# Kernel tuning notes

Hardware: AMD Instinct MI355X
Metric: run time of the kernel (lower is better)

## Reference

```python
import jax, jax.numpy as jnp
import numpy as np

N_QUBITS = 10
BATCH = 16384
Q_DEPTH = 2


def _apply_1q_shared(state, U, q):
    # state: [B, 2, 2, ..., 2]; U: [2, 2] complex, acting on wire q
    state = jnp.moveaxis(state, 1 + q, -1)
    state = jnp.einsum('b...i,ji->b...j', state, U)
    return jnp.moveaxis(state, -1, 1 + q)


def _apply_ry_batched(state, angles, q):
    # per-sample RY(angle) on wire q; angles: [B] float
    c = jnp.cos(angles * 0.5).astype(jnp.complex64)
    s = jnp.sin(angles * 0.5).astype(jnp.complex64)
    U = jnp.stack([jnp.stack([c, -s], -1), jnp.stack([s, c], -1)], -2)  # [B,2,2]
    state = jnp.moveaxis(state, 1 + q, -1)
    state = jnp.einsum('b...i,bji->b...j', state, U)
    return jnp.moveaxis(state, -1, 1 + q)


def _rot_matrix(phi, theta, omega):
    # PennyLane Rot = RZ(omega) @ RY(theta) @ RZ(phi)
    c = jnp.cos(theta * 0.5)
    s = jnp.sin(theta * 0.5)
    m00 = jnp.exp(-0.5j * (phi + omega)) * c
    m01 = -jnp.exp(0.5j * (phi - omega)) * s
    m10 = jnp.exp(-0.5j * (phi - omega)) * s
    m11 = jnp.exp(0.5j * (phi + omega)) * c
    return jnp.stack([jnp.stack([m00, m01]), jnp.stack([m10, m11])]).astype(jnp.complex64)


def _apply_cnot(state, c, t):
    st = jnp.moveaxis(state, (1 + c, 1 + t), (1, 2))  # [B, ctrl, tgt, ...]
    st = jnp.stack([st[:, 0], st[:, 1, ::-1]], axis=1)  # flip target where ctrl=1
    return jnp.moveaxis(st, (1, 2), (1 + c, 1 + t))


def setup_inputs() -> dict:
    key = jax.random.key(0)
    k1, k2 = jax.random.split(key)
    x = jax.random.uniform(k1, (BATCH, N_QUBITS), dtype=jnp.float32) * np.pi
    q_weights = 0.01 * jax.random.normal(k2, (Q_DEPTH, N_QUBITS, 3), dtype=jnp.float32)
    return {"x": x, "q_weights": q_weights}


def reference(x, q_weights) -> jnp.ndarray:
    B, n = x.shape
    L = q_weights.shape[0]
    # |0...0> statevector, batched: [B] + [2]*n (axis q <-> wire q, wire 0 most significant)
    state = jnp.zeros((B, 2 ** n), jnp.complex64).at[:, 0].set(1.0)
    state = state.reshape((B,) + (2,) * n)
    # AngleEmbedding(rotation='Y')
    for q in range(n):
        state = _apply_ry_batched(state, x[:, q], q)
    # StronglyEntanglingLayers: Rot on each wire, then ring of CNOTs with range (l % (n-1)) + 1
    for l in range(L):
        for q in range(n):
            U = _rot_matrix(q_weights[l, q, 0], q_weights[l, q, 1], q_weights[l, q, 2])
            state = _apply_1q_shared(state, U, q)
        r = (l % (n - 1)) + 1
        for q in range(n):
            state = _apply_cnot(state, q, (q + r) % n)
    probs = jnp.abs(state.reshape(B, 2 ** n)) ** 2  # [B, 2^n]
    bits = (np.arange(2 ** n)[:, None] >> (n - 1 - np.arange(n))[None, :]) & 1
    signs = jnp.asarray(1.0 - 2.0 * bits, jnp.float32)  # [2^n, n], PauliZ eigenvalues
    return (probs @ signs).astype(jnp.float32)  # [B, n] expvals
```

## Files before the change

### kernel.cpp

```cpp
#include <hip/hip_runtime.h>

#define DEVINL __device__ __forceinline__

struct GC { int laneXor, regXor, rowL, rowR; };
struct Circ { GC g[20]; int sgnL[10], sgnR[10]; };

constexpr Circ build_circ() {
    Circ c{};
    unsigned A[10] = {};
    for (int i = 0; i < 10; ++i) A[i] = 1u << i;
    for (int w = 0; w < 10; ++w) {
        int pos = 9 - w;
        unsigned m = 1u << pos;
        c.g[w] = GC{ int(m >> 4), int(m & 15u), int(m >> 4), int(m & 15u) };
    }
    for (int q = 0; q < 10; ++q) { int pc = 9 - q, pt = 9 - ((q + 1) % 10); A[pt] ^= A[pc]; }
    unsigned M[10] = {}, Inv[10] = {};
    for (int i = 0; i < 10; ++i) { M[i] = A[i]; Inv[i] = 1u << i; }
    for (int col = 0; col < 10; ++col) {
        int piv = col;
        while (!((M[piv] >> col) & 1u)) ++piv;
        unsigned tm = M[col]; M[col] = M[piv]; M[piv] = tm;
        unsigned ti = Inv[col]; Inv[col] = Inv[piv]; Inv[piv] = ti;
        for (int r = 0; r < 10; ++r)
            if (r != col && ((M[r] >> col) & 1u)) { M[r] ^= M[col]; Inv[r] ^= Inv[col]; }
    }
    for (int w = 0; w < 10; ++w) {
        int pos = 9 - w;
        unsigned m = 0;
        for (int i = 0; i < 10; ++i) m |= ((Inv[i] >> pos) & 1u) << i;
        unsigned row = A[pos];
        c.g[10 + w] = GC{ int(m >> 4), int(m & 15u), int(row >> 4), int(row & 15u) };
    }
    for (int q = 0; q < 10; ++q) { int pc = 9 - q, pt = 9 - ((q + 2) % 10); A[pt] ^= A[pc]; }
    for (int q = 0; q < 10; ++q) { unsigned row = A[9 - q]; c.sgnL[q] = int(row >> 4); c.sgnR[q] = int(row & 15u); }
    return c;
}

constexpr Circ CC = build_circ();

DEVINL float csign(float v, int s) {
    return __int_as_float(__float_as_int(v) ^ (s << 31));
}

template<int XOR>
DEVINL float lx(float v, int lane) {
    int x = __float_as_int(v);
    int r;
    if constexpr (XOR == 1)      r = __builtin_amdgcn_update_dpp(0, x, 0xB1, 0xF, 0xF, true);
    else if constexpr (XOR == 2) r = __builtin_amdgcn_update_dpp(0, x, 0x4E, 0xF, 0xF, true);
    else if constexpr (XOR == 3) r = __builtin_amdgcn_update_dpp(0, x, 0x1B, 0xF, 0xF, true);
    else if constexpr (XOR < 32) r = __builtin_amdgcn_ds_swizzle(x, 0x1F | (XOR << 10));
    else                         r = __builtin_amdgcn_ds_bpermute((lane ^ XOR) << 2, x);
    return __int_as_float(r);
}

template<int G>
DEVINL void gates(float (&ar)[16], float (&ai)[16], const float* mats, int lane) {
    if constexpr (G < 20) {
        constexpr GC gc = CC.g[G];
        float fAr = mats[G * 4 + 0];
        float fAi = mats[G * 4 + 1];
        float fBr = mats[G * 4 + 2];
        float fBi = mats[G * 4 + 3];
        int sL = __popc(unsigned(lane & gc.rowL)) & 1;
        fAi = csign(fAi, sL);
        fBr = csign(fBr, sL);
        float br_[16], bi_[16];
        if constexpr (gc.laneXor == 0) {
            #pragma unroll
            for (int r = 0; r < 16; ++r) { br_[r] = ar[r ^ gc.regXor]; bi_[r] = ai[r ^ gc.regXor]; }
        } else {
            #pragma unroll
            for (int r = 0; r < 16; ++r) {
                br_[r] = lx<gc.laneXor>(ar[r ^ gc.regXor], lane);
                bi_[r] = lx<gc.laneXor>(ai[r ^ gc.regXor], lane);
            }
        }
        #pragma unroll
        for (int r = 0; r < 16; ++r) {
            const int cR = __builtin_popcount(unsigned(gc.rowR & r)) & 1;
            float a_r = ar[r], a_i = ai[r], b_r = br_[r], b_i = bi_[r];
            float nr, ni;
            if (!cR) {
                nr = fAr * a_r - fAi * a_i + fBr * b_r - fBi * b_i;
                ni = fAr * a_i + fAi * a_r + fBr * b_i + fBi * b_r;
            } else {
                nr = fAr * a_r + fAi * a_i - fBr * b_r - fBi * b_i;
                ni = fAr * a_i - fAi * a_r - fBr * b_i + fBi * b_r;
            }
            ar[r] = nr; ai[r] = ni;
        }
        gates<G + 1>(ar, ai, mats, lane);
    }
}

__global__ __launch_bounds__(256) void qsim(const float* __restrict__ x,
                                            const float* __restrict__ qw,
                                            float* __restrict__ out, int B) {
    __shared__ float sm[80];
    {
        int g = threadIdx.x;
        if (g < 20) {
            float phi = qw[g * 3 + 0], th = qw[g * 3 + 1], om = qw[g * 3 + 2];
            float c = cosf(0.5f * th), s = sinf(0.5f * th);
            float apo = 0.5f * (phi + om), amo = 0.5f * (phi - om);
            sm[g * 4 + 0] =  cosf(apo) * c;
            sm[g * 4 + 1] = -sinf(apo) * c;
            sm[g * 4 + 2] = -cosf(amo) * s;
            sm[g * 4 + 3] = -sinf(amo) * s;
        }
    }
    __syncthreads();

    int lane = threadIdx.x & 63;
    int b = __builtin_amdgcn_readfirstlane(blockIdx.x * 4 + (threadIdx.x >> 6));
    if (b >= B) return;

    const float* xb = x + b * 10;
    float f0r[10], f0i[10], f1r[10], f1i[10];
    #pragma unroll
    for (int w = 0; w < 10; ++w) {
        float h = 0.5f * xb[w];
        float s = __sinf(h), c = __cosf(h);
        float m0 = sm[w * 4 + 0], m1 = sm[w * 4 + 1], m2 = sm[w * 4 + 2], m3 = sm[w * 4 + 3];
        f0r[w] =  m0 * c + m2 * s;
        f0i[w] =  m1 * c + m3 * s;
        f1r[w] = -m2 * c + m0 * s;
        f1i[w] =  m3 * c - m1 * s;
    }

    float lfr, lfi;
    {
        int bit = lane & 1;
        lfr = bit ? f1r[5] : f0r[5];
        lfi = bit ? f1i[5] : f0i[5];
    }
    #pragma unroll
    for (int jj = 1; jj < 6; ++jj) {
        int w = 5 - jj;
        int bit = (lane >> jj) & 1;
        float pr = bit ? f1r[w] : f0r[w];
        float pi = bit ? f1i[w] : f0i[w];
        float nr = lfr * pr - lfi * pi;
        float ni = lfr * pi + lfi * pr;
        lfr = nr; lfi = ni;
    }
    float t01r[4], t01i[4], t23r[4], t23i[4];
    #pragma unroll
    for (int v = 0; v < 4; ++v) {
        float ar9 = (v & 1) ? f1r[9] : f0r[9], ai9 = (v & 1) ? f1i[9] : f0i[9];
        float ar8 = (v >> 1) ? f1r[8] : f0r[8], ai8 = (v >> 1) ? f1i[8] : f0i[8];
        t01r[v] = ar9 * ar8 - ai9 * ai8;
        t01i[v] = ar9 * ai8 + ai9 * ar8;
        float ar7 = (v & 1) ? f1r[7] : f0r[7], ai7 = (v & 1) ? f1i[7] : f0i[7];
        float ar6 = (v >> 1) ? f1r[6] : f0r[6], ai6 = (v >> 1) ? f1i[6] : f0i[6];
        t23r[v] = ar7 * ar6 - ai7 * ai6;
        t23i[v] = ar7 * ai6 + ai7 * ar6;
    }
    float g4r[4], g4i[4];
    #pragma unroll
    for (int v = 0; v < 4; ++v) {
        g4r[v] = lfr * t01r[v] - lfi * t01i[v];
        g4i[v] = lfr * t01i[v] + lfi * t01r[v];
    }
    float ar[16], ai[16];
    #pragma unroll
    for (int r = 0; r < 16; ++r) {
        ar[r] = g4r[r & 3] * t23r[r >> 2] - g4i[r & 3] * t23i[r >> 2];
        ai[r] = g4r[r & 3] * t23i[r >> 2] + g4i[r & 3] * t23r[r >> 2];
    }

    gates<10>(ar, ai, sm, lane);

    float prob[16];
    #pragma unroll
    for (int r = 0; r < 16; ++r) prob[r] = ar[r] * ar[r] + ai[r] * ai[r];

    float e[10];
    #pragma unroll
    for (int q = 0; q < 10; ++q) {
        float t = 0.f;
        #pragma unroll
        for (int r = 0; r < 16; ++r) {
            const int neg = __builtin_popcount(unsigned(CC.sgnR[q] & r)) & 1;
            t = neg ? (t - prob[r]) : (t + prob[r]);
        }
        int sl = __popc(unsigned(lane & CC.sgnL[q])) & 1;
        e[q] = csign(t, sl);
    }
    #pragma unroll
    for (int q = 0; q < 10; ++q) {
        e[q] += lx<1>(e[q], lane);
        e[q] += lx<2>(e[q], lane);
        e[q] += lx<4>(e[q], lane);
        e[q] += lx<8>(e[q], lane);
        e[q] += lx<16>(e[q], lane);
        e[q] += lx<32>(e[q], lane);
    }
    float v = e[0];
    #pragma unroll
    for (int q = 1; q < 10; ++q) v = (lane == q) ? e[q] : v;
    if (lane < 10) out[b * 10 + lane] = v;
}

extern "C" void kernel_launch(void* const* d_in, const int* in_sizes, int n_in,
                              void* d_out, int out_size, void* d_ws, size_t ws_size,
                              hipStream_t stream) {
    const float* x  = (const float*)d_in[0];
    const float* qw = (const float*)d_in[1];
    float* out = (float*)d_out;
    int B = in_sizes[0] / 10;
    int blocks = (B + 3) / 4;
    hipLaunchKernelGGL(qsim, dim3(blocks), dim3(256), 0, stream, x, qw, out, B);
}
```

Baseline: 95.30 us.

## Pack statevector amplitudes as fp16 pairs and apply gates with fdot2

```diff
diff --git a/kernel.cpp b/kernel.cpp
--- a/kernel.cpp
+++ b/kernel.cpp
@@ -1,6 +1,8 @@
 #include <hip/hip_runtime.h>
 
 #define DEVINL __device__ __forceinline__
+
+typedef _Float16 h2_t __attribute__((ext_vector_type(2)));
 
 struct GC { int laneXor, regXor, rowL, rowR; };
 struct Circ { GC g[20]; int sgnL[10], sgnR[10]; };
@@ -43,72 +45,79 @@
     return __int_as_float(__float_as_int(v) ^ (s << 31));
 }
 
+DEVINL int pk(float a, float b) {
+    return __builtin_bit_cast(int, __builtin_amdgcn_cvt_pkrtz(a, b));
+}
+DEVINL float fdot2(int p, int v, float acc) {
+    return __builtin_amdgcn_fdot2(__builtin_bit_cast(h2_t, p), __builtin_bit_cast(h2_t, v), acc, false);
+}
+
 template<int XOR>
-DEVINL float lx(float v, int lane) {
-    int x = __float_as_int(v);
-    int r;
-    if constexpr (XOR == 1)      r = __builtin_amdgcn_update_dpp(0, x, 0xB1, 0xF, 0xF, true);
-    else if constexpr (XOR == 2) r = __builtin_amdgcn_update_dpp(0, x, 0x4E, 0xF, 0xF, true);
-    else if constexpr (XOR == 3) r = __builtin_amdgcn_update_dpp(0, x, 0x1B, 0xF, 0xF, true);
-    else if constexpr (XOR < 32) r = __builtin_amdgcn_ds_swizzle(x, 0x1F | (XOR << 10));
-    else                         r = __builtin_amdgcn_ds_bpermute((lane ^ XOR) << 2, x);
-    return __int_as_float(r);
+DEVINL int lxi(int x, int lane) {
+    if constexpr (XOR == 1)      return __builtin_amdgcn_update_dpp(0, x, 0xB1, 0xF, 0xF, true);
+    else if constexpr (XOR == 2) return __builtin_amdgcn_update_dpp(0, x, 0x4E, 0xF, 0xF, true);
+    else if constexpr (XOR == 3) return __builtin_amdgcn_update_dpp(0, x, 0x1B, 0xF, 0xF, true);
+    else if constexpr (XOR < 32) return __builtin_amdgcn_ds_swizzle(x, 0x1F | (XOR << 10));
+    else                         return __builtin_amdgcn_ds_bpermute((lane ^ XOR) << 2, x);
+}
+template<int XOR>
+DEVINL float lxf(float v, int lane) {
+    return __int_as_float(lxi<XOR>(__float_as_int(v), lane));
 }
 
 template<int G>
-DEVINL void gates(float (&ar)[16], float (&ai)[16], const float* mats, int lane) {
+DEVINL void gates(int (&a)[16], const int* smP, int lane) {
     if constexpr (G < 20) {
         constexpr GC gc = CC.g[G];
-        float fAr = mats[G * 4 + 0];
-        float fAi = mats[G * 4 + 1];
-        float fBr = mats[G * 4 + 2];
-        float fBi = mats[G * 4 + 3];
         int sL = __popc(unsigned(lane & gc.rowL)) & 1;
-        fAi = csign(fAi, sL);
-        fBr = csign(fBr, sL);
-        float br_[16], bi_[16];
+        int p1 = smP[G * 4 + 0] ^ (sL << 31);
+        int p2 = smP[G * 4 + 1] ^ (sL << 15);
+        int p3 = smP[G * 4 + 2] ^ (sL << 15);
+        int p4 = smP[G * 4 + 3] ^ (sL << 31);
+        int q1 = p1 ^ (int)0x80000000;
+        int q2 = p2 ^ 0x8000;
+        int q3 = p3 ^ 0x8000;
+        int q4 = p4 ^ (int)0x80000000;
+        int b_[16];
         if constexpr (gc.laneXor == 0) {
             #pragma unroll
-            for (int r = 0; r < 16; ++r) { br_[r] = ar[r ^ gc.regXor]; bi_[r] = ai[r ^ gc.regXor]; }
+            for (int r = 0; r < 16; ++r) b_[r] = a[r ^ gc.regXor];
         } else {
             #pragma unroll
-            for (int r = 0; r < 16; ++r) {
-                br_[r] = lx<gc.laneXor>(ar[r ^ gc.regXor], lane);
-                bi_[r] = lx<gc.laneXor>(ai[r ^ gc.regXor], lane);
-            }
+            for (int r = 0; r < 16; ++r) b_[r] = lxi<gc.laneXor>(a[r ^ gc.regXor], lane);
         }
         #pragma unroll
         for (int r = 0; r < 16; ++r) {
             const int cR = __builtin_popcount(unsigned(gc.rowR & r)) & 1;
-            float a_r = ar[r], a_i = ai[r], b_r = br_[r], b_i = bi_[r];
-            float nr, ni;
-            if (!cR) {
-                nr = fAr * a_r - fAi * a_i + fBr * b_r - fBi * b_i;
-                ni = fAr * a_i + fAi * a_r + fBr * b_i + fBi * b_r;
-            } else {
-                nr = fAr * a_r + fAi * a_i - fBr * b_r - fBi * b_i;
-                ni = fAr * a_i - fAi * a_r - fBr * b_i + fBi * b_r;
-            }
-            ar[r] = nr; ai[r] = ni;
-        }
-        gates<G + 1>(ar, ai, mats, lane);
+            float nr = fdot2(cR ? q1 : p1, a[r], fdot2(cR ? q2 : p2, b_[r], 0.f));
+            float ni = fdot2(cR ? q3 : p3, a[r], fdot2(cR ? q4 : p4, b_[r], 0.f));
+            a[r] = pk(nr, ni);
+        }
+        gates<G + 1>(a, smP, lane);
     }
 }
 
 __global__ __launch_bounds__(256) void qsim(const float* __restrict__ x,
                                             const float* __restrict__ qw,
                                             float* __restrict__ out, int B) {
-    __shared__ float sm[80];
+    __shared__ float sm32[80];
+    __shared__ int smP[80];
     {
         int g = threadIdx.x;
         if (g < 20) {
             float phi = qw[g * 3 + 0], th = qw[g * 3 + 1], om = qw[g * 3 + 2];
             float c = cosf(0.5f * th), s = sinf(0.5f * th);
             float apo = 0.5f * (phi + om), amo = 0.5f * (phi - om);
-            sm[g * 4 + 0] =  cosf(apo) * c;
-            sm[g * 4 + 1] = -sinf(apo) * c;
-            sm[g * 4 + 2] = -cosf(amo) * s;
-            sm[g * 4 + 3] = -sinf(amo) * s;
+            float m0 =  cosf(apo) * c;
+            float m1 = -sinf(apo) * c;
+            float m2 = -cosf(amo) * s;
+            float m3 = -sinf(amo) * s;
+            sm32[g * 4 + 0] = m0; sm32[g * 4 + 1] = m1;
+            sm32[g * 4 + 2] = m2; sm32[g * 4 + 3] = m3;
+            smP[g * 4 + 0] = pk(m0, -m1);
+            smP[g * 4 + 1] = pk(m2, -m3);
+            smP[g * 4 + 2] = pk(m1,  m0);
+            smP[g * 4 + 3] = pk(m3,  m2);
         }
     }
     __syncthreads();
@@ -123,13 +132,12 @@
     for (int w = 0; w < 10; ++w) {
         float h = 0.5f * xb[w];
         float s = __sinf(h), c = __cosf(h);
-        float m0 = sm[w * 4 + 0], m1 = sm[w * 4 + 1], m2 = sm[w * 4 + 2], m3 = sm[w * 4 + 3];
+        float m0 = sm32[w * 4 + 0], m1 = sm32[w * 4 + 1], m2 = sm32[w * 4 + 2], m3 = sm32[w * 4 + 3];
         f0r[w] =  m0 * c + m2 * s;
         f0i[w] =  m1 * c + m3 * s;
         f1r[w] = -m2 * c + m0 * s;
         f1i[w] =  m3 * c - m1 * s;
     }
-
     float lfr, lfi;
     {
         int bit = lane & 1;
@@ -164,39 +172,44 @@
         g4r[v] = lfr * t01r[v] - lfi * t01i[v];
         g4i[v] = lfr * t01i[v] + lfi * t01r[v];
     }
-    float ar[16], ai[16];
+    int a[16];
     #pragma unroll
     for (int r = 0; r < 16; ++r) {
-        ar[r] = g4r[r & 3] * t23r[r >> 2] - g4i[r & 3] * t23i[r >> 2];
-        ai[r] = g4r[r & 3] * t23i[r >> 2] + g4i[r & 3] * t23r[r >> 2];
-    }
-
-    gates<10>(ar, ai, sm, lane);
-
-    float prob[16];
-    #pragma unroll
-    for (int r = 0; r < 16; ++r) prob[r] = ar[r] * ar[r] + ai[r] * ai[r];
-
+        float ar = g4r[r & 3] * t23r[r >> 2] - g4i[r & 3] * t23i[r >> 2];
+        float ai = g4r[r & 3] * t23i[r >> 2] + g4i[r & 3] * t23r[r >> 2];
+        a[r] = pk(ar, ai);
+    }
+
+    gates<10>(a, smP, lane);
+
+    float t[16];
+    #pragma unroll
+    for (int r = 0; r < 16; ++r) t[r] = fdot2(a[r], a[r], 0.f);
+    #pragma unroll
+    for (int bit = 1; bit < 16; bit <<= 1) {
+        #pragma unroll
+        for (int i = 0; i < 16; ++i) {
+            if ((i & bit) == 0) {
+                float u = t[i], v = t[i | bit];
+                t[i] = u + v;
+                t[i | bit] = u - v;
+            }
+        }
+    }
     float e[10];
     #pragma unroll
     for (int q = 0; q < 10; ++q) {
-        float t = 0.f;
-        #pragma unroll
-        for (int r = 0; r < 16; ++r) {
-            const int neg = __builtin_popcount(unsigned(CC.sgnR[q] & r)) & 1;
-            t = neg ? (t - prob[r]) : (t + prob[r]);
-        }
         int sl = __popc(unsigned(lane & CC.sgnL[q])) & 1;
-        e[q] = csign(t, sl);
+        e[q] = csign(t[CC.sgnR[q]], sl);
     }
     #pragma unroll
     for (int q = 0; q < 10; ++q) {
-        e[q] += lx<1>(e[q], lane);
-        e[q] += lx<2>(e[q], lane);
-        e[q] += lx<4>(e[q], lane);
-        e[q] += lx<8>(e[q], lane);
-        e[q] += lx<16>(e[q], lane);
-        e[q] += lx<32>(e[q], lane);
+        e[q] += lxf<1>(e[q], lane);
+        e[q] += lxf<2>(e[q], lane);
+        e[q] += lxf<4>(e[q], lane);
+        e[q] += lxf<8>(e[q], lane);
+        e[q] += lxf<16>(e[q], lane);
+        e[q] += lxf<32>(e[q], lane);
     }
     float v = e[0];
     #pragma unroll
```

New measurement: 99.08 us. 4.0% more time.
